# Kernel optimization log

Hardware: AMD Instinct MI355X
Metric: run time of the kernel (lower is better)

The kernel has to match this reference:

```python
import jax, jax.numpy as jnp
import numpy as np

D = 768
NH = 8
HD = D // NH
DFF = 2048
EPS = 1e-5


def _layer_norm(x, g, b):
    mu = jnp.mean(x, axis=-1, keepdims=True)
    var = jnp.mean(jnp.square(x - mu), axis=-1, keepdims=True)
    return (x - mu) * jax.lax.rsqrt(var + EPS) * g + b


def setup_inputs() -> dict:
    key = jax.random.key(0)
    ks = jax.random.split(key, 16)
    B, L = 2, 2048
    s = 0.02
    return {
        "x": jax.random.normal(ks[0], (B, L, D), jnp.float32),
        "attn_bias": jax.random.normal(ks[1], (B, L, L), jnp.float32),
        "in_proj_w": jax.random.normal(ks[2], (3 * D, D), jnp.float32) * s,
        "in_proj_b": jnp.zeros((3 * D,), jnp.float32),
        "out_w": jax.random.normal(ks[3], (D, D), jnp.float32) * s,
        "out_b": jnp.zeros((D,), jnp.float32),
        "W1": jax.random.normal(ks[4], (DFF, D), jnp.float32) * s,
        "b1": jnp.zeros((DFF,), jnp.float32),
        "W2": jax.random.normal(ks[5], (D, DFF), jnp.float32) * s,
        "b2": jnp.zeros((D,), jnp.float32),
        "g1": jnp.ones((D,), jnp.float32),
        "be1": jnp.zeros((D,), jnp.float32),
        "g2": jnp.ones((D,), jnp.float32),
        "be2": jnp.zeros((D,), jnp.float32),
    }


def reference(x, attn_bias, in_proj_w, in_proj_b, out_w, out_b,
              W1, b1, W2, b2, g1, be1, g2, be2):
    B, L, _ = x.shape
    # fused qkv projection (torch nn.MultiheadAttention in_proj)
    qkv = x @ in_proj_w.T + in_proj_b          # [B, L, 3D]
    q, k, v = jnp.split(qkv, 3, axis=-1)
    q = q.reshape(B, L, NH, HD).transpose(0, 2, 1, 3)  # [B, nH, L, hd]
    k = k.reshape(B, L, NH, HD).transpose(0, 2, 1, 3)
    v = v.reshape(B, L, NH, HD).transpose(0, 2, 1, 3)
    scale = 1.0 / jnp.sqrt(jnp.asarray(HD, x.dtype))
    scores = jnp.einsum("bhqd,bhkd->bhqk", q * scale, k)
    scores = scores + attn_bias[:, None, :, :]         # broadcast over heads == expand
    attn = jax.nn.softmax(scores, axis=-1)
    ctx = jnp.einsum("bhqk,bhkd->bhqd", attn, v)       # [B, nH, L, hd]
    ctx = ctx.transpose(0, 2, 1, 3).reshape(B, L, D)
    attn_out = ctx @ out_w.T + out_b
    x = _layer_norm(x + attn_out, g1, be1)
    h = jax.nn.gelu(x @ W1.T + b1, approximate=False)  # torch default GELU = erf
    ff = h @ W2.T + b2
    return _layer_norm(x + ff, g2, be2)
```

## Files before the change

kernel.cpp:

```cpp
#include <hip/hip_runtime.h>
#include <hip/hip_bf16.h>
#include <math.h>

typedef __bf16 bf16;
typedef __attribute__((ext_vector_type(8))) __bf16 bf16x8;
typedef __attribute__((ext_vector_type(4))) __bf16 bf16x4;
typedef __attribute__((ext_vector_type(4))) float f32x4;

#define LOG2E 1.4426950408889634f

__global__ void cast_kernel(const float* __restrict__ src, bf16* __restrict__ dst, int n4) {
  int i = blockIdx.x * blockDim.x + threadIdx.x;
  int stride = gridDim.x * blockDim.x;
  for (; i < n4; i += stride) {
    float4 v = ((const float4*)src)[i];
    bf16x4 o = { (bf16)v.x, (bf16)v.y, (bf16)v.z, (bf16)v.w };
    ((bf16x4*)dst)[i] = o;
  }
}

template<int MODE>
__launch_bounds__(256)
__global__ void gemm_kernel(const bf16* __restrict__ A, const bf16* __restrict__ W,
                            const float* __restrict__ bias, const float* __restrict__ res,
                            void* __restrict__ out, int K, int O) {
  __shared__ bf16 As[128][80];
  __shared__ bf16 Bs[128][80];
  const int t    = threadIdx.x;
  const int lane = t & 63;
  const int wave = t >> 6;
  const int wr = (wave >> 1) * 64;
  const int wc = (wave & 1) * 64;
  const int n0 = blockIdx.y * 128;
  const int o0 = blockIdx.x * 128;

  f32x4 zero = {0.f, 0.f, 0.f, 0.f};
  f32x4 acc[4][4];
#pragma unroll
  for (int m = 0; m < 4; m++)
#pragma unroll
    for (int n = 0; n < 4; n++) acc[m][n] = zero;

  const int r_l = t >> 3;
  const int c_l = (t & 7) * 8;
  const int fr  = lane & 15;
  const int fg8 = (lane >> 4) * 8;

  for (int k0 = 0; k0 < K; k0 += 64) {
    __syncthreads();
#pragma unroll
    for (int j = 0; j < 4; j++) {
      int row = r_l + 32 * j;
      *(bf16x8*)&As[row][c_l] = *(const bf16x8*)&A[(size_t)(n0 + row) * K + k0 + c_l];
      *(bf16x8*)&Bs[row][c_l] = *(const bf16x8*)&W[(size_t)(o0 + row) * K + k0 + c_l];
    }
    __syncthreads();
#pragma unroll
    for (int kf = 0; kf < 2; kf++) {
      bf16x8 a[4], b[4];
#pragma unroll
      for (int m = 0; m < 4; m++) a[m] = *(const bf16x8*)&As[wr + m * 16 + fr][kf * 32 + fg8];
#pragma unroll
      for (int n = 0; n < 4; n++) b[n] = *(const bf16x8*)&Bs[wc + n * 16 + fr][kf * 32 + fg8];
#pragma unroll
      for (int m = 0; m < 4; m++)
#pragma unroll
        for (int n = 0; n < 4; n++)
          acc[m][n] = __builtin_amdgcn_mfma_f32_16x16x32_bf16(a[m], b[n], acc[m][n], 0, 0, 0);
    }
  }

  const int fg4 = (lane >> 4) * 4;
#pragma unroll
  for (int m = 0; m < 4; m++) {
#pragma unroll
    for (int n = 0; n < 4; n++) {
      int col = o0 + wc + n * 16 + fr;
      float bv = bias[col];
#pragma unroll
      for (int r = 0; r < 4; r++) {
        int row = n0 + wr + m * 16 + fg4 + r;
        float v = acc[m][n][r] + bv;
        if constexpr (MODE == 1) {
          v += res[(size_t)row * O + col];
          ((float*)out)[(size_t)row * O + col] = v;
        } else if constexpr (MODE == 2) {
          v = 0.5f * v * (1.0f + erff(v * 0.70710678118654752f));
          ((bf16*)out)[(size_t)row * O + col] = (bf16)v;
        } else {
          ((bf16*)out)[(size_t)row * O + col] = (bf16)v;
        }
      }
    }
  }
}

__launch_bounds__(256)
__global__ void attn_kernel(const bf16* __restrict__ qkv, const float* __restrict__ bias,
                            bf16* __restrict__ ctx) {
  __shared__ bf16 Ks[64][120];
  __shared__ bf16 Vt[96][80];
  __shared__ bf16 Pl[4][16][80];
  const int t    = threadIdx.x;
  const int lane = t & 63;
  const int wave = t >> 6;
  const int qb = blockIdx.x;
  const int h  = blockIdx.y;
  const int b  = blockIdx.z;
  const int L  = 2048;
  const size_t base = (size_t)b * L * 2304;
  const int q0 = qb * 64 + wave * 16;
  const int fq = lane & 15;
  const int g  = lane >> 4;

  bf16x8 qf[3];
  {
    const bf16* qp = qkv + base + (size_t)(q0 + fq) * 2304 + h * 96;
#pragma unroll
    for (int f = 0; f < 3; f++) qf[f] = *(const bf16x8*)(qp + f * 32 + g * 8);
  }

  float m_run = -1e30f, l_run = 0.f;
  f32x4 zero = {0.f, 0.f, 0.f, 0.f};
  f32x4 o_acc[6];
#pragma unroll
  for (int i = 0; i < 6; i++) o_acc[i] = zero;

  const float scale = 0.10206207261596575f;
  const float* bp = bias + ((size_t)b * L + (q0 + fq)) * L;

  const int kvr  = t & 63;
  const int offb = (t >> 6) * 8;

  for (int kv0 = 0; kv0 < L; kv0 += 64) {
    __syncthreads();
    {
      const bf16* kp = qkv + base + (size_t)(kv0 + kvr) * 2304 + 768 + h * 96;
      const bf16* vp = kp + 768;
#pragma unroll
      for (int i = 0; i < 3; i++) {
        int off = offb + 32 * i;
        *(bf16x8*)&Ks[kvr][off] = *(const bf16x8*)(kp + off);
        bf16x8 vv = *(const bf16x8*)(vp + off);
#pragma unroll
        for (int j = 0; j < 8; j++) Vt[off + j][kvr] = vv[j];
      }
    }
    __syncthreads();

    f32x4 s[4];
#pragma unroll
    for (int kvt = 0; kvt < 4; kvt++) {
      s[kvt] = zero;
#pragma unroll
      for (int f = 0; f < 3; f++) {
        bf16x8 kfr = *(const bf16x8*)&Ks[kvt * 16 + fq][f * 32 + g * 8];
        s[kvt] = __builtin_amdgcn_mfma_f32_16x16x32_bf16(kfr, qf[f], s[kvt], 0, 0, 0);
      }
    }

    float p[4][4];
    float vmax = -1e30f;
#pragma unroll
    for (int kvt = 0; kvt < 4; kvt++) {
      float4 bv = *(const float4*)(bp + kv0 + kvt * 16 + g * 4);
#pragma unroll
      for (int r = 0; r < 4; r++) {
        float sv = s[kvt][r] * scale + (&bv.x)[r];
        p[kvt][r] = sv;
        vmax = fmaxf(vmax, sv);
      }
    }
    vmax = fmaxf(vmax, __shfl_xor(vmax, 16));
    vmax = fmaxf(vmax, __shfl_xor(vmax, 32));
    float m_new = fmaxf(m_run, vmax);
    float corr = exp2f((m_run - m_new) * LOG2E);
    float rsum = 0.f;
#pragma unroll
    for (int kvt = 0; kvt < 4; kvt++) {
      bf16x4 pb;
#pragma unroll
      for (int r = 0; r < 4; r++) {
        float pv = exp2f((p[kvt][r] - m_new) * LOG2E);
        rsum += pv;
        pb[r] = (bf16)pv;
      }
      *(bf16x4*)&Pl[wave][fq][kvt * 16 + g * 4] = pb;
    }
    rsum += __shfl_xor(rsum, 16);
    rsum += __shfl_xor(rsum, 32);
    l_run = l_run * corr + rsum;
    m_run = m_new;
#pragma unroll
    for (int i = 0; i < 6; i++)
#pragma unroll
      for (int r = 0; r < 4; r++) o_acc[i][r] *= corr;
    __syncthreads();

#pragma unroll
    for (int kf = 0; kf < 2; kf++) {
      bf16x8 pfrag = *(const bf16x8*)&Pl[wave][fq][kf * 32 + g * 8];
#pragma unroll
      for (int ht = 0; ht < 6; ht++) {
        bf16x8 vfrag = *(const bf16x8*)&Vt[ht * 16 + fq][kf * 32 + g * 8];
        o_acc[ht] = __builtin_amdgcn_mfma_f32_16x16x32_bf16(vfrag, pfrag, o_acc[ht], 0, 0, 0);
      }
    }
  }

  float inv = 1.0f / l_run;
  bf16* cp = ctx + ((size_t)b * L + (q0 + fq)) * 768 + h * 96;
#pragma unroll
  for (int ht = 0; ht < 6; ht++) {
    bf16x4 ov;
#pragma unroll
    for (int r = 0; r < 4; r++) ov[r] = (bf16)(o_acc[ht][r] * inv);
    *(bf16x4*)(cp + ht * 16 + g * 4) = ov;
  }
}

__launch_bounds__(256)
__global__ void ln_kernel(const float* in, const float* __restrict__ gamma,
                          const float* __restrict__ beta, float* outf, bf16* outb) {
  const int row = blockIdx.x;
  const int t = threadIdx.x;
  const float* rp = in + (size_t)row * 768;
  float v[3];
#pragma unroll
  for (int i = 0; i < 3; i++) v[i] = rp[t + 256 * i];
  float s = v[0] + v[1] + v[2];
  float ss = v[0] * v[0] + v[1] * v[1] + v[2] * v[2];
#pragma unroll
  for (int off = 1; off < 64; off <<= 1) {
    s += __shfl_xor(s, off);
    ss += __shfl_xor(ss, off);
  }
  __shared__ float red[8];
  if ((t & 63) == 0) { red[(t >> 6) * 2] = s; red[(t >> 6) * 2 + 1] = ss; }
  __syncthreads();
  s = red[0] + red[2] + red[4] + red[6];
  ss = red[1] + red[3] + red[5] + red[7];
  float mu = s * (1.0f / 768.0f);
  float var = ss * (1.0f / 768.0f) - mu * mu;
  float rs = rsqrtf(var + 1e-5f);
#pragma unroll
  for (int i = 0; i < 3; i++) {
    int col = t + 256 * i;
    float y = (v[i] - mu) * rs * gamma[col] + beta[col];
    outf[(size_t)row * 768 + col] = y;
    if (outb) outb[(size_t)row * 768 + col] = (bf16)y;
  }
}

extern "C" void kernel_launch(void* const* d_in, const int* in_sizes, int n_in,
                              void* d_out, int out_size, void* d_ws, size_t ws_size,
                              hipStream_t stream) {
  (void)in_sizes; (void)n_in; (void)out_size; (void)ws_size;
  const float* x     = (const float*)d_in[0];
  const float* ab    = (const float*)d_in[1];
  const float* w_qkv = (const float*)d_in[2];
  const float* b_qkv = (const float*)d_in[3];
  const float* w_out = (const float*)d_in[4];
  const float* b_out = (const float*)d_in[5];
  const float* W1    = (const float*)d_in[6];
  const float* b1    = (const float*)d_in[7];
  const float* W2    = (const float*)d_in[8];
  const float* b2    = (const float*)d_in[9];
  const float* g1    = (const float*)d_in[10];
  const float* be1   = (const float*)d_in[11];
  const float* g2    = (const float*)d_in[12];
  const float* be2   = (const float*)d_in[13];
  float* outf = (float*)d_out;

  char* p = (char*)d_ws;
  bf16* xb    = (bf16*)p;  p += (size_t)4096 * 768 * 2;
  bf16* qkv   = (bf16*)p;  p += (size_t)4096 * 2304 * 2;
  bf16* ctx   = (bf16*)p;  p += (size_t)4096 * 768 * 2;
  float* x1f  = (float*)p; p += (size_t)4096 * 768 * 4;
  bf16* x1b   = (bf16*)p;  p += (size_t)4096 * 768 * 2;
  bf16* hbuf  = (bf16*)p;  p += (size_t)4096 * 2048 * 2;
  bf16* wqkvb = (bf16*)p;  p += (size_t)2304 * 768 * 2;
  bf16* woutb = (bf16*)p;  p += (size_t)768 * 768 * 2;
  bf16* w1b   = (bf16*)p;  p += (size_t)2048 * 768 * 2;
  bf16* w2b   = (bf16*)p;  p += (size_t)768 * 2048 * 2;

  cast_kernel<<<1024, 256, 0, stream>>>(x, xb, 4096 * 768 / 4);
  cast_kernel<<<512, 256, 0, stream>>>(w_qkv, wqkvb, 2304 * 768 / 4);
  cast_kernel<<<256, 256, 0, stream>>>(w_out, woutb, 768 * 768 / 4);
  cast_kernel<<<512, 256, 0, stream>>>(W1, w1b, 2048 * 768 / 4);
  cast_kernel<<<512, 256, 0, stream>>>(W2, w2b, 768 * 2048 / 4);

  gemm_kernel<0><<<dim3(18, 32), 256, 0, stream>>>(xb, wqkvb, b_qkv, nullptr, qkv, 768, 2304);
  attn_kernel<<<dim3(32, 8, 2), 256, 0, stream>>>(qkv, ab, ctx);
  gemm_kernel<1><<<dim3(6, 32), 256, 0, stream>>>(ctx, woutb, b_out, x, outf, 768, 768);
  ln_kernel<<<4096, 256, 0, stream>>>(outf, g1, be1, x1f, x1b);
  gemm_kernel<2><<<dim3(16, 32), 256, 0, stream>>>(x1b, w1b, b1, nullptr, hbuf, 768, 2048);
  gemm_kernel<1><<<dim3(6, 32), 256, 0, stream>>>(hbuf, w2b, b2, x1f, outf, 2048, 768);
  ln_kernel<<<4096, 256, 0, stream>>>(outf, g2, be2, outf, nullptr);
}
```

Before: 259.6 us.

## Pipeline attention K/V loads, pre-transpose V, bf16 bias, direct-to-LDS GEMM loads

```diff
diff --git a/kernel.cpp b/kernel.cpp
--- a/kernel.cpp
+++ b/kernel.cpp
@@ -8,6 +8,12 @@
 typedef __attribute__((ext_vector_type(4))) float f32x4;
 
 #define LOG2E 1.4426950408889634f
+
+__device__ __forceinline__ void gload16(const bf16* g, bf16* l) {
+  __builtin_amdgcn_global_load_lds(
+      (const __attribute__((address_space(1))) void*)g,
+      (__attribute__((address_space(3))) void*)l, 16, 0, 0);
+}
 
 __global__ void cast_kernel(const float* __restrict__ src, bf16* __restrict__ dst, int n4) {
   int i = blockIdx.x * blockDim.x + threadIdx.x;
@@ -19,13 +25,38 @@
   }
 }
 
+__launch_bounds__(256)
+__global__ void vtrans_kernel(const bf16* __restrict__ qkv, bf16* __restrict__ vt) {
+  __shared__ bf16 T[96][72];
+  const int t = threadIdx.x;
+  const int tk0 = blockIdx.x * 64;
+  const int h = blockIdx.y, b = blockIdx.z;
+  const bf16* vp = qkv + ((size_t)b * 2048 + tk0) * 2304 + 1536 + h * 96;
+  const int row = t >> 2;
+  const int cb = (t & 3) * 24;
+#pragma unroll
+  for (int i = 0; i < 3; i++) {
+    bf16x8 v = *(const bf16x8*)(vp + (size_t)row * 2304 + cb + i * 8);
+#pragma unroll
+    for (int j = 0; j < 8; j++) T[cb + i * 8 + j][row] = v[j];
+  }
+  __syncthreads();
+  bf16* op = vt + (size_t)((b * 8 + h) * 96) * 2048 + tk0;
+#pragma unroll
+  for (int i = 0; i < 3; i++) {
+    int hd = (t >> 3) + i * 32;
+    int tk = (t & 7) * 8;
+    *(bf16x8*)(op + (size_t)hd * 2048 + tk) = *(const bf16x8*)&T[hd][tk];
+  }
+}
+
 template<int MODE>
 __launch_bounds__(256)
 __global__ void gemm_kernel(const bf16* __restrict__ A, const bf16* __restrict__ W,
                             const float* __restrict__ bias, const float* __restrict__ res,
                             void* __restrict__ out, int K, int O) {
-  __shared__ bf16 As[128][80];
-  __shared__ bf16 Bs[128][80];
+  __shared__ bf16 As[128 * 64];
+  __shared__ bf16 Bs[128 * 64];
   const int t    = threadIdx.x;
   const int lane = t & 63;
   const int wave = t >> 6;
@@ -41,27 +72,27 @@
 #pragma unroll
     for (int n = 0; n < 4; n++) acc[m][n] = zero;
 
-  const int r_l = t >> 3;
-  const int c_l = (t & 7) * 8;
   const int fr  = lane & 15;
   const int fg8 = (lane >> 4) * 8;
 
   for (int k0 = 0; k0 < K; k0 += 64) {
     __syncthreads();
 #pragma unroll
-    for (int j = 0; j < 4; j++) {
-      int row = r_l + 32 * j;
-      *(bf16x8*)&As[row][c_l] = *(const bf16x8*)&A[(size_t)(n0 + row) * K + k0 + c_l];
-      *(bf16x8*)&Bs[row][c_l] = *(const bf16x8*)&W[(size_t)(o0 + row) * K + k0 + c_l];
+    for (int c = 0; c < 4; c++) {
+      int f = c * 256 + t;
+      int row = f >> 3;
+      int col = (f & 7) * 8;
+      gload16(&A[(size_t)(n0 + row) * K + k0 + col], &As[f * 8]);
+      gload16(&W[(size_t)(o0 + row) * K + k0 + col], &Bs[f * 8]);
     }
     __syncthreads();
 #pragma unroll
     for (int kf = 0; kf < 2; kf++) {
       bf16x8 a[4], b[4];
 #pragma unroll
-      for (int m = 0; m < 4; m++) a[m] = *(const bf16x8*)&As[wr + m * 16 + fr][kf * 32 + fg8];
-#pragma unroll
-      for (int n = 0; n < 4; n++) b[n] = *(const bf16x8*)&Bs[wc + n * 16 + fr][kf * 32 + fg8];
+      for (int m = 0; m < 4; m++) a[m] = *(const bf16x8*)&As[(wr + m * 16 + fr) * 64 + kf * 32 + fg8];
+#pragma unroll
+      for (int n = 0; n < 4; n++) b[n] = *(const bf16x8*)&Bs[(wc + n * 16 + fr) * 64 + kf * 32 + fg8];
 #pragma unroll
       for (int m = 0; m < 4; m++)
 #pragma unroll
@@ -95,23 +126,20 @@
   }
 }
 
-__launch_bounds__(256)
-__global__ void attn_kernel(const bf16* __restrict__ qkv, const float* __restrict__ bias,
-                            bf16* __restrict__ ctx) {
-  __shared__ bf16 Ks[64][120];
-  __shared__ bf16 Vt[96][80];
-  __shared__ bf16 Pl[4][16][80];
+__launch_bounds__(512, 2)
+__global__ void attn_kernel(const bf16* __restrict__ qkv, const bf16* __restrict__ vt,
+                            const bf16* __restrict__ biasb, bf16* __restrict__ ctx) {
+  __shared__ bf16 Ks[2][64][104];
+  __shared__ bf16 Vs[2][96][72];
+  __shared__ bf16 Pl[8][16][72];
   const int t    = threadIdx.x;
   const int lane = t & 63;
   const int wave = t >> 6;
-  const int qb = blockIdx.x;
-  const int h  = blockIdx.y;
-  const int b  = blockIdx.z;
-  const int L  = 2048;
-  const size_t base = (size_t)b * L * 2304;
-  const int q0 = qb * 64 + wave * 16;
+  const int qb = blockIdx.x, h = blockIdx.y, b = blockIdx.z;
+  const int q0 = qb * 128 + wave * 16;
   const int fq = lane & 15;
   const int g  = lane >> 4;
+  const size_t base = (size_t)b * 2048 * 2304;
 
   bf16x8 qf[3];
   {
@@ -120,6 +148,24 @@
     for (int f = 0; f < 3; f++) qf[f] = *(const bf16x8*)(qp + f * 32 + g * 8);
   }
 
+  const int kr1 = t >> 3, kc1 = (t & 7) * 8;
+  const int kr2 = t >> 2, kc2 = 64 + (t & 3) * 8;
+  const int vr2 = 64 + (t >> 3);
+  const bf16* kbase = qkv + base + 768 + h * 96;
+  const bf16* vbase = vt + (size_t)((b * 8 + h) * 96) * 2048;
+
+  bf16x8 kreg0, kreg1, vreg0, vreg1;
+  const bool lo = (t < 256);
+
+  {
+    kreg0 = *(const bf16x8*)(kbase + (size_t)kr1 * 2304 + kc1);
+    vreg0 = *(const bf16x8*)(vbase + (size_t)kr1 * 2048 + kc1);
+    if (lo) {
+      kreg1 = *(const bf16x8*)(kbase + (size_t)kr2 * 2304 + kc2);
+      vreg1 = *(const bf16x8*)(vbase + (size_t)vr2 * 2048 + kc1);
+    }
+  }
+
   float m_run = -1e30f, l_run = 0.f;
   f32x4 zero = {0.f, 0.f, 0.f, 0.f};
   f32x4 o_acc[6];
@@ -127,26 +173,32 @@
   for (int i = 0; i < 6; i++) o_acc[i] = zero;
 
   const float scale = 0.10206207261596575f;
-  const float* bp = bias + ((size_t)b * L + (q0 + fq)) * L;
-
-  const int kvr  = t & 63;
-  const int offb = (t >> 6) * 8;
-
-  for (int kv0 = 0; kv0 < L; kv0 += 64) {
+  const bf16* bp = biasb + ((size_t)b * 2048 + q0 + fq) * 2048;
+
+  int cur = 0;
+  for (int kv0 = 0; kv0 < 2048; kv0 += 64) {
+    *(bf16x8*)&Ks[cur][kr1][kc1] = kreg0;
+    *(bf16x8*)&Vs[cur][kr1][kc1] = vreg0;
+    if (lo) {
+      *(bf16x8*)&Ks[cur][kr2][kc2] = kreg1;
+      *(bf16x8*)&Vs[cur][vr2][kc1] = vreg1;
+    }
     __syncthreads();
-    {
-      const bf16* kp = qkv + base + (size_t)(kv0 + kvr) * 2304 + 768 + h * 96;
-      const bf16* vp = kp + 768;
-#pragma unroll
-      for (int i = 0; i < 3; i++) {
-        int off = offb + 32 * i;
-        *(bf16x8*)&Ks[kvr][off] = *(const bf16x8*)(kp + off);
-        bf16x8 vv = *(const bf16x8*)(vp + off);
-#pragma unroll
-        for (int j = 0; j < 8; j++) Vt[off + j][kvr] = vv[j];
-      }
-    }
-    __syncthreads();
+
+    if (kv0 + 64 < 2048) {
+      int nx = kv0 + 64;
+      kreg0 = *(const bf16x8*)(kbase + (size_t)(nx + kr1) * 2304 + kc1);
+      vreg0 = *(const bf16x8*)(vbase + (size_t)kr1 * 2048 + nx + kc1);
+      if (lo) {
+        kreg1 = *(const bf16x8*)(kbase + (size_t)(nx + kr2) * 2304 + kc2);
+        vreg1 = *(const bf16x8*)(vbase + (size_t)vr2 * 2048 + nx + kc1);
+      }
+    }
+
+    bf16x4 bb[4];
+#pragma unroll
+    for (int kvt = 0; kvt < 4; kvt++)
+      bb[kvt] = *(const bf16x4*)(bp + kv0 + kvt * 16 + g * 4);
 
     f32x4 s[4];
 #pragma unroll
@@ -154,7 +206,7 @@
       s[kvt] = zero;
 #pragma unroll
       for (int f = 0; f < 3; f++) {
-        bf16x8 kfr = *(const bf16x8*)&Ks[kvt * 16 + fq][f * 32 + g * 8];
+        bf16x8 kfr = *(const bf16x8*)&Ks[cur][kvt * 16 + fq][f * 32 + g * 8];
         s[kvt] = __builtin_amdgcn_mfma_f32_16x16x32_bf16(kfr, qf[f], s[kvt], 0, 0, 0);
       }
     }
@@ -163,25 +215,32 @@
     float vmax = -1e30f;
 #pragma unroll
     for (int kvt = 0; kvt < 4; kvt++) {
-      float4 bv = *(const float4*)(bp + kv0 + kvt * 16 + g * 4);
 #pragma unroll
       for (int r = 0; r < 4; r++) {
-        float sv = s[kvt][r] * scale + (&bv.x)[r];
+        float sv = s[kvt][r] * scale + (float)bb[kvt][r];
         p[kvt][r] = sv;
         vmax = fmaxf(vmax, sv);
       }
     }
     vmax = fmaxf(vmax, __shfl_xor(vmax, 16));
     vmax = fmaxf(vmax, __shfl_xor(vmax, 32));
-    float m_new = fmaxf(m_run, vmax);
-    float corr = exp2f((m_run - m_new) * LOG2E);
+    if (!__all(vmax <= m_run + 8.0f)) {
+      float m_new = fmaxf(m_run, vmax);
+      float corr = exp2f((m_run - m_new) * LOG2E);
+      l_run *= corr;
+#pragma unroll
+      for (int i = 0; i < 6; i++)
+#pragma unroll
+        for (int r = 0; r < 4; r++) o_acc[i][r] *= corr;
+      m_run = m_new;
+    }
     float rsum = 0.f;
 #pragma unroll
     for (int kvt = 0; kvt < 4; kvt++) {
       bf16x4 pb;
 #pragma unroll
       for (int r = 0; r < 4; r++) {
-        float pv = exp2f((p[kvt][r] - m_new) * LOG2E);
+        float pv = exp2f((p[kvt][r] - m_run) * LOG2E);
         rsum += pv;
         pb[r] = (bf16)pv;
       }
@@ -189,27 +248,22 @@
     }
     rsum += __shfl_xor(rsum, 16);
     rsum += __shfl_xor(rsum, 32);
-    l_run = l_run * corr + rsum;
-    m_run = m_new;
-#pragma unroll
-    for (int i = 0; i < 6; i++)
-#pragma unroll
-      for (int r = 0; r < 4; r++) o_acc[i][r] *= corr;
-    __syncthreads();
+    l_run += rsum;
 
 #pragma unroll
     for (int kf = 0; kf < 2; kf++) {
       bf16x8 pfrag = *(const bf16x8*)&Pl[wave][fq][kf * 32 + g * 8];
 #pragma unroll
       for (int ht = 0; ht < 6; ht++) {
-        bf16x8 vfrag = *(const bf16x8*)&Vt[ht * 16 + fq][kf * 32 + g * 8];
+        bf16x8 vfrag = *(const bf16x8*)&Vs[cur][ht * 16 + fq][kf * 32 + g * 8];
         o_acc[ht] = __builtin_amdgcn_mfma_f32_16x16x32_bf16(vfrag, pfrag, o_acc[ht], 0, 0, 0);
       }
     }
+    cur ^= 1;
   }
 
   float inv = 1.0f / l_run;
-  bf16* cp = ctx + ((size_t)b * L + (q0 + fq)) * 768 + h * 96;
+  bf16* cp = ctx + ((size_t)b * 2048 + q0 + fq) * 768 + h * 96;
 #pragma unroll
   for (int ht = 0; ht < 6; ht++) {
     bf16x4 ov;
@@ -283,15 +337,19 @@
   bf16* woutb = (bf16*)p;  p += (size_t)768 * 768 * 2;
   bf16* w1b   = (bf16*)p;  p += (size_t)2048 * 768 * 2;
   bf16* w2b   = (bf16*)p;  p += (size_t)768 * 2048 * 2;
+  bf16* vtb   = (bf16*)x1f;
+  bf16* biasb = hbuf;
 
   cast_kernel<<<1024, 256, 0, stream>>>(x, xb, 4096 * 768 / 4);
   cast_kernel<<<512, 256, 0, stream>>>(w_qkv, wqkvb, 2304 * 768 / 4);
   cast_kernel<<<256, 256, 0, stream>>>(w_out, woutb, 768 * 768 / 4);
   cast_kernel<<<512, 256, 0, stream>>>(W1, w1b, 2048 * 768 / 4);
   cast_kernel<<<512, 256, 0, stream>>>(W2, w2b, 768 * 2048 / 4);
+  cast_kernel<<<2048, 256, 0, stream>>>(ab, biasb, 2 * 2048 * 2048 / 4);
 
   gemm_kernel<0><<<dim3(18, 32), 256, 0, stream>>>(xb, wqkvb, b_qkv, nullptr, qkv, 768, 2304);
-  attn_kernel<<<dim3(32, 8, 2), 256, 0, stream>>>(qkv, ab, ctx);
+  vtrans_kernel<<<dim3(32, 8, 2), 256, 0, stream>>>(qkv, vtb);
+  attn_kernel<<<dim3(16, 8, 2), 512, 0, stream>>>(qkv, vtb, biasb, ctx);
   gemm_kernel<1><<<dim3(6, 32), 256, 0, stream>>>(ctx, woutb, b_out, x, outf, 768, 768);
   ln_kernel<<<4096, 256, 0, stream>>>(outf, g1, be1, x1f, x1b);
   gemm_kernel<2><<<dim3(16, 32), 256, 0, stream>>>(x1b, w1b, b1, nullptr, hbuf, 768, 2048);
```

Result: no change. 264.1 us (+1.7%).
